# Kernel tuning notes

Hardware: AMD Instinct MI355X
Metric: run time of the kernel (lower is better)

The kernel has to match this reference:

```python
import math
import jax, jax.numpy as jnp
import numpy as np
from jax.scipy.linalg import cho_factor, cho_solve, block_diag

NUM_SENSORS = 64
T_STEPS = 2048
LOG2PI = float(np.log(2.0 * np.pi))

NCV_PROCESS_NOISE = np.array([[1.0/3.0, 0.0, 0.5, 0.0],
                              [0.0, 1.0/3.0, 0.0, 0.5],
                              [0.5, 0.0, 1.0, 0.0],
                              [0.0, 0.5, 0.0, 1.0]], dtype=np.float32)
NCV_TRANSITION_MATRIX = np.array([[1.0, 0.0, 1.0, 0.0],
                                  [0.0, 1.0, 0.0, 1.0],
                                  [0.0, 0.0, 1.0, 0.0],
                                  [0.0, 0.0, 0.0, 1.0]], dtype=np.float32)


def setup_inputs() -> dict:
    key = jax.random.key(0)
    k1, k2 = jax.random.split(key)
    track = jax.random.normal(k1, (T_STEPS, 2), dtype=jnp.float32)
    # positive covariance scales for the bias prior (torch param init ~ ones)
    bias_scales = jax.random.uniform(k2, (2,), jnp.float32, 0.5, 1.5)
    obs_noise = jnp.float32(0.7)
    trans_noise = jnp.float32(0.3)
    return {"track": track, "bias_scales": bias_scales,
            "obs_noise": obs_noise, "trans_noise": trans_noise}


def _hmm_forward(track, bias_scales, obs_noise, trans_noise, num_sensors):
    S = num_sensors
    OD = 2 * S           # obs_dim
    D = OD + 4           # augmented latent: [bias(OD); state(4)]
    T = track.shape[0]
    dt = track.dtype

    # observation matrix exactly as in torch source:
    # eye(4,2).expand(S,4,2).transpose(0,-1).reshape(4, OD)
    E = jnp.eye(4, 2, dtype=dt)
    Hobs = jnp.transpose(jnp.broadcast_to(E, (S, 4, 2)), (2, 1, 0)).reshape(4, OD)
    # augmented emission: y = bias + state @ Hobs  ->  H_aug z
    Haug = jnp.concatenate([jnp.eye(OD, dtype=dt), Hobs.T], axis=1)  # (OD, D)

    F = jnp.asarray(NCV_TRANSITION_MATRIX, dt)
    # trans scale_tril = trans_noise * chol(NCV_Q) -> cov = trans_noise^2 * NCV_Q
    Qs = (trans_noise ** 2) * jnp.asarray(NCV_PROCESS_NOISE, dt)
    A = block_diag(jnp.eye(OD, dtype=dt), F)                         # (D, D)
    Q = block_diag(jnp.zeros((OD, OD), dt), Qs)                      # (D, D)
    # obs scale_tril = obs_noise * I -> cov = obs_noise^2 * I
    R = (obs_noise ** 2) * jnp.eye(OD, dtype=dt)

    # bias prior covariance = diag(bias_scales interleaved per sensor)
    bias_var = jnp.broadcast_to(bias_scales, (S, 2)).reshape(-1)     # (OD,)
    m0 = jnp.zeros((D,), dt)
    P0 = jnp.diag(jnp.concatenate([bias_var, jnp.ones((4,), dt)]))

    # obs vector per step: x.expand(S,2).reshape(-1) (interleaved repeat)
    ys = jnp.broadcast_to(track[:, None, :], (T, S, 2)).reshape(T, OD)

    def step(carry, y):
        m, P, ll = carry
        # predict
        mp = A @ m
        Pp = A @ P @ A.T + Q
        # innovation
        HP = Haug @ Pp                      # (OD, D)
        Sm = HP @ Haug.T + R                # (OD, OD)
        cf = cho_factor(Sm, lower=True)
        v = y - Haug @ mp                   # (OD,)
        # update
        K = cho_solve(cf, HP)               # S^{-1} H Pp, (OD, D)
        m_new = mp + K.T @ v
        P_new = Pp - HP.T @ K
        P_new = 0.5 * (P_new + P_new.T)
        # log-likelihood of innovation
        logdet = 2.0 * jnp.sum(jnp.log(jnp.diag(cf[0])))
        quad = v @ cho_solve(cf, v)
        ll = ll - 0.5 * (OD * LOG2PI + logdet + quad)
        return (m_new, P_new, ll), None

    (mT, PT, ll), _ = jax.lax.scan(step, (m0, P0, jnp.zeros((), dt)), ys)
    # funsor's remaining Gaussian over (bias, state_T) has precision = inv(filtered cov)
    cfP = cho_factor(PT, lower=True)
    prec = cho_solve(cfP, jnp.eye(D, dtype=dt))
    return ll, prec


def reference(track, bias_scales, obs_noise, trans_noise):
    return _hmm_forward(track, bias_scales, obs_noise, trans_noise, NUM_SENSORS)
```

## Files before the change

kernel.cpp:

```cpp
#include <hip/hip_runtime.h>
#include <math.h>

#define L2PI 1.8378770664093454835606594728112
#define LN2  0.69314718055994530941723212145818

struct LP {
    float jFF, jFL, jFB, jLL, jLB, jBB;
    float hF, hL, hB, g, dm, de;
};

struct Cn { float qa, qb, qc, wa, wb, ri, Cstep; };

__device__ __forceinline__ float shf(float v, int s) { return __shfl(v, s, 64); }
__device__ __forceinline__ float sx (float v, int m) { return __shfl_xor(v, m, 64); }

#define LGKM0() do { \
    asm volatile("s_waitcnt lgkmcnt(0)" ::: "memory"); \
    __builtin_amdgcn_sched_barrier(0); \
} while (0)

#define OFF_S   0
#define OFF_SI  16
#define OFF_F1  32
#define OFF_F2T 48
#define OFF_MT  64
#define OFF_A1  80
#define OFF_C1T 96
#define OFF_B2T 112
#define OFF_V4  128
#define OFF_HM  132
#define GSTRIDE 152

__device__ __forceinline__ float4 ld4(const float* p) {
    return *(const float4*)p;
}
__device__ __forceinline__ float dot4(float4 a, float4 b) {
    float s = a.x * b.x;
    s = fmaf(a.y, b.y, s);
    s = fmaf(a.z, b.z, s);
    s = fmaf(a.w, b.w, s);
    return s;
}

__device__ __forceinline__ LP init_lane(float x0, float x1, const Cn& C, int i, int j) {
    LP P;
    float v = 0.0f;
    if (i == j) v = (i < 2) ? C.qa : C.qc;
    if ((i ^ j) == 2) v = C.wa;
    P.jFF = v;
    v = 0.0f;
    if (j == (i & 1))     v = (i < 2) ? -C.qa : -C.wa;
    if (j == (i & 1) + 2) v = (i < 2) ? -C.qb : -C.wb;
    P.jFL = v;
    P.jFB = 0.0f;
    v = 0.0f;
    if (i == j) v = ((i < 2) ? C.qa : C.qc) + (((i & 1) == 0) ? 2.0f*C.ri : 0.0f);
    if ((i ^ j) == 2) v = C.qb;
    P.jLL = v;
    P.jLB = (((i == 0) && (j < 2)) || ((i == 2) && (j >= 2))) ? C.ri : 0.0f;
    P.jBB = (i == j) ? C.ri : 0.0f;
    P.hF = 0.0f;
    P.hL = ((j & 1) == 0) ? C.ri * (x0 + x1) : 0.0f;
    P.hB = C.ri * ((j & 1) ? x1 : x0);
    P.g  = -C.ri * (x0*x0 + x1*x1) + C.Cstep;
    P.dm = 1.0f; P.de = 0.0f;
    return P;
}

__device__ __forceinline__ LP compose(const LP& P1, const LP& P2, float* gl, int i, int j) {
    float hm = P1.hL + P2.hF;
    float Mb = P1.jLB + P2.jFB;
    float S  = P1.jLL + P2.jFF;
    float dm = P1.dm * P2.dm;
    float de = P1.de + P2.de;
    { int ex; dm = frexpf(dm, &ex); de += (float)ex; }
    const int ij = 4*i + j, ji = 4*j + i;

    gl[OFF_S   + ij] = S;
    gl[OFF_F1  + ij] = P1.jFL;
    gl[OFF_F2T + ji] = P2.jFL;
    gl[OFF_MT  + ji] = Mb;
    if (i == 0) gl[OFF_HM + j] = hm;
    LGKM0();

    const int r0 = (j == 0) ? 1 : 0;
    const int r1 = (j <= 1) ? 2 : 1;
    const int r2 = (j <= 2) ? 3 : 2;
    float4 R0 = ld4(gl + OFF_S + 4*r0);
    float4 R1 = ld4(gl + OFF_S + 4*r1);
    float4 R2 = ld4(gl + OFF_S + 4*r2);
    float4 RJ = ld4(gl + OFF_S + 4*j);
    float4 f1r4 = ld4(gl + OFF_F1  + 4*i);
    float4 f1T4 = ld4(gl + OFF_F1  + 4*j);
    float4 f2c4 = ld4(gl + OFF_F2T + 4*j);
    float4 f2T4 = ld4(gl + OFF_F2T + 4*i);
    float4 mc4  = ld4(gl + OFF_MT  + 4*j);
    float4 mT4  = ld4(gl + OFF_MT  + 4*i);
    float4 hm4  = ld4(gl + OFF_HM);

    const bool i0 = (i == 0), i1 = (i <= 1), i2 = (i <= 2);
    float m00 = i0 ? R0.y : R0.x, m01 = i1 ? R0.z : R0.y, m02 = i2 ? R0.w : R0.z;
    float m10 = i0 ? R1.y : R1.x, m11 = i1 ? R1.z : R1.y, m12 = i2 ? R1.w : R1.z;
    float m20 = i0 ? R2.y : R2.x, m21 = i1 ? R2.z : R2.y, m22 = i2 ? R2.w : R2.z;
    float d0 = fmaf(m11, m22, -m12*m21);
    float d1 = fmaf(m10, m22, -m12*m20);
    float d2 = fmaf(m10, m21, -m11*m20);
    float det3 = m00*d0 - m01*d1 + m02*d2;
    float adj = (((i + j) & 1) ? -det3 : det3);
    float sji = (i < 2) ? (i0 ? RJ.x : RJ.y) : ((i == 2) ? RJ.z : RJ.w);
    float t = sji * adj;
    t += sx(t, 4); t += sx(t, 8);
    float det = t;
    dm *= det; { int ex; dm = frexpf(dm, &ex); de += (float)ex; }
    float Sio = adj * (1.0f / det);

    gl[OFF_SI + ij] = Sio;
    LGKM0();
    float4 sr4 = ld4(gl + OFF_SI + 4*i);
    float4 sc4 = ld4(gl + OFF_SI + 4*j);

    float A1  = dot4(f1r4, sc4);
    float C1  = dot4(sr4,  mc4);
    float B2  = dot4(sr4,  f2c4);
    float v4i = dot4(sr4,  hm4);

    gl[OFF_A1  + ij] = A1;
    gl[OFF_C1T + ji] = C1;
    gl[OFF_B2T + ji] = B2;
    if (i == j) gl[OFF_V4 + i] = v4i;
    LGKM0();
    float4 a1r4 = ld4(gl + OFF_A1  + 4*i);
    float4 a1j4 = ld4(gl + OFF_A1  + 4*j);
    float4 c1c4 = ld4(gl + OFF_C1T + 4*j);
    float4 b2c4 = ld4(gl + OFF_B2T + 4*j);
    float4 v44  = ld4(gl + OFF_V4);

    LP R;
    R.jFF = P1.jFF - dot4(a1r4, f1T4);
    R.jFL = -dot4(a1r4, f2c4);
    R.jFB = P1.jFB - dot4(a1r4, mc4);
    R.jLL = P2.jLL - dot4(f2T4, b2c4);
    R.jLB = P2.jLB - dot4(f2T4, c1c4);
    R.jBB = P1.jBB + P2.jBB - dot4(mT4, c1c4);
    R.hF  = P1.hF - dot4(a1j4, hm4);
    R.hL  = P2.hL - dot4(f2c4, v44);
    R.hB  = P1.hB + P2.hB - dot4(mc4, v44);
    R.g   = P1.g + P2.g + 2.0f*(float)L2PI + 0.5f*dot4(hm4, v44);
    R.dm = dm; R.de = de;
    return R;
}

__device__ __forceinline__ LP fetchx(const LP& P, int m) {
    LP O;
    O.jFF = sx(P.jFF,m); O.jFL = sx(P.jFL,m); O.jFB = sx(P.jFB,m);
    O.jLL = sx(P.jLL,m); O.jLB = sx(P.jLB,m); O.jBB = sx(P.jBB,m);
    O.hF  = sx(P.hF,m);  O.hL  = sx(P.hL,m);  O.hB  = sx(P.hB,m);
    O.g   = sx(P.g,m);   O.dm  = sx(P.dm,m);  O.de  = sx(P.de,m);
    return O;
}
__device__ __forceinline__ LP csel(bool up, const LP& O, const LP& P) {
    LP A;
    A.jFF = up?O.jFF:P.jFF; A.jFL = up?O.jFL:P.jFL; A.jFB = up?O.jFB:P.jFB;
    A.jLL = up?O.jLL:P.jLL; A.jLB = up?O.jLB:P.jLB; A.jBB = up?O.jBB:P.jBB;
    A.hF  = up?O.hF :P.hF;  A.hL  = up?O.hL :P.hL;  A.hB  = up?O.hB :P.hB;
    A.g   = up?O.g  :P.g;   A.dm  = up?O.dm :P.dm;  A.de  = up?O.de :P.de;
    return A;
}
__device__ __forceinline__ void pot_store(float* p, const LP& P) {
    p[0]=P.jFF; p[1]=P.jFL; p[2]=P.jFB; p[3]=P.jLL; p[4]=P.jLB; p[5]=P.jBB;
    p[6]=P.hF;  p[7]=P.hL;  p[8]=P.hB;  p[9]=P.g;   p[10]=P.dm; p[11]=P.de;
}
__device__ __forceinline__ LP pot_load(const float* p) {
    LP P;
    P.jFF=p[0]; P.jFL=p[1]; P.jFB=p[2]; P.jLL=p[3]; P.jLB=p[4]; P.jBB=p[5];
    P.hF=p[6];  P.hL=p[7];  P.hB=p[8];  P.g=p[9];   P.dm=p[10]; P.de=p[11];
    return P;
}

__global__ __launch_bounds__(512)
void hmm_produce(const float* __restrict__ track,
                 const float* __restrict__ obs_noise_p,
                 const float* __restrict__ trans_noise_p,
                 float* __restrict__ ws)
{
    __shared__ float pool[2][8][16][13];
    __shared__ __align__(16) float cbuf[32 * GSTRIDE];
    const int tid = (int)threadIdx.x;
    const int l = tid & 63, w = tid >> 6;
    const int i = (l >> 2) & 3, j = l & 3, g = (l >> 4) & 3;
    const int gid = w * 4 + g;
    float* gl = &cbuf[(size_t)gid * GSTRIDE];
    const int bid = (int)blockIdx.x;

    const double sg2d = (double)obs_noise_p[0] * (double)obs_noise_p[0];
    const double qn2d = (double)trans_noise_p[0] * (double)trans_noise_p[0];

    Cn C;
    C.qa = (float)(12.0/qn2d); C.qb = (float)(-6.0/qn2d); C.qc = (float)(4.0/qn2d);
    C.wa = (float)(6.0/qn2d);  C.wb = (float)(-2.0/qn2d);
    C.ri = (float)(32.0/sg2d);
    C.Cstep = (float)(-2.0*log(2.0*M_PI*sg2d/32.0) - 2.0*L2PI
                      - 0.5*(4.0*log(qn2d) - 2.0*log(12.0)));

    const int t0 = (bid * 32 + gid) * 2;
    LP P;
    #pragma unroll 1
    for (int op = 0; op < 6; ++op) {
        LP A, Bp;
        if (op == 0) {
            A  = init_lane(track[2*t0+0], track[2*t0+1], C, i, j);
            Bp = init_lane(track[2*t0+2], track[2*t0+3], C, i, j);
        } else if (op < 3) {
            const int m = 16 << (op - 1);
            LP O = fetchx(P, m);
            const bool up = (l & m) != 0;
            A  = csel(up, O, P);
            Bp = csel(up, P, O);
        } else {
            const int s = 1 << (op - 3);
            const int buf = (op - 3) & 1;
            if (l < 16) pot_store(&pool[buf][w][l][0], P);
            __syncthreads();
            LP O = pot_load(&pool[buf][w ^ s][l & 15][0]);
            const bool up = (w & s) != 0;
            A  = csel(up, O, P);
            Bp = csel(up, P, O);
        }
        P = compose(A, Bp, gl, i, j);
    }
    if (w == 0 && l < 16)
        pot_store(ws + ((size_t)bid * 16 + l) * 12, P);
}

__global__ __launch_bounds__(512)
void hmm_consume(const float* __restrict__ bias_scales,
                 const float* __restrict__ obs_noise_p,
                 const float* __restrict__ ws,
                 float* __restrict__ out)
{
    __shared__ float pool[2][8][16][13];
    __shared__ __align__(16) float cbuf[32 * GSTRIDE];
    __shared__ float sTi[8][8];
    __shared__ float sA[4];
    __shared__ float sLL;
    const int tid = (int)threadIdx.x;
    const int l = tid & 63, w = tid >> 6;
    const int i = (l >> 2) & 3, j = l & 3, gb = l & 48, g = (l >> 4) & 3;
    const int gid = w * 4 + g;
    float* gl = &cbuf[(size_t)gid * GSTRIDE];

    const double sg2d = (double)obs_noise_p[0] * (double)obs_noise_p[0];
    const double a00 = (double)bias_scales[0];
    const double a01 = (double)bias_scales[1];

    LP P = pot_load(ws + ((size_t)gid * 16 + (l & 15)) * 12);
    #pragma unroll 1
    for (int op = 0; op < 5; ++op) {
        LP A, Bp;
        if (op < 2) {
            const int m = 16 << op;
            LP O = fetchx(P, m);
            const bool up = (l & m) != 0;
            A  = csel(up, O, P);
            Bp = csel(up, P, O);
        } else {
            const int s = 1 << (op - 2);
            const int buf = (op - 2) & 1;
            if (l < 16) pot_store(&pool[buf][w][l][0], P);
            __syncthreads();
            LP O = pot_load(&pool[buf][w ^ s][l & 15][0]);
            const bool up = (w & s) != 0;
            A  = csel(up, O, P);
            Bp = csel(up, P, O);
        }
        P = compose(A, Bp, gl, i, j);
    }

    if (w == 0) {
        const float a0i = (float)((i & 1) ? a01 : a00);
        P.jFF += (i == j) ? 1.0f : 0.0f;
        P.jBB += (i == j) ? 32.0f / a0i : 0.0f;
        P.g   += (float)(-4.0*L2PI + 2.0*log(32.0) - log(a00) - log(a01));
        float dm = P.dm, de = P.de;
        float S = P.jFF;
        const int r0 = (j == 0) ? 1 : 0;
        const int r1 = (j <= 1) ? 2 : 1;
        const int r2 = (j <= 2) ? 3 : 2;
        const int c0 = (i == 0) ? 1 : 0;
        const int c1 = (i <= 1) ? 2 : 1;
        const int c2 = (i <= 2) ? 3 : 2;
        float m00 = shf(S, gb + 4*r0 + c0), m01 = shf(S, gb + 4*r0 + c1), m02 = shf(S, gb + 4*r0 + c2);
        float m10 = shf(S, gb + 4*r1 + c0), m11 = shf(S, gb + 4*r1 + c1), m12 = shf(S, gb + 4*r1 + c2);
        float m20 = shf(S, gb + 4*r2 + c0), m21 = shf(S, gb + 4*r2 + c1), m22 = shf(S, gb + 4*r2 + c2);
        float d0 = fmaf(m11, m22, -m12*m21);
        float d1 = fmaf(m10, m22, -m12*m20);
        float d2 = fmaf(m10, m21, -m11*m20);
        float det3 = m00*d0 - m01*d1 + m02*d2;
        float adj = (((i + j) & 1) ? -det3 : det3);
        float sji = shf(S, gb + 4*j + i);
        float tdet = sji * adj;
        tdet += sx(tdet, 4); tdet += sx(tdet, 8);
        float det = tdet;
        dm *= det; { int ex; dm = frexpf(dm, &ex); de += (float)ex; }
        const float Si = adj * (1.0f / det);
        float sr[4], fr[4], fT[4], bc[4], bT[4], hfc[4];
        #pragma unroll
        for (int r = 0; r < 4; ++r) {
            sr[r]  = shf(Si, gb + 4*i + r);
            fr[r]  = shf(P.jFL, gb + 4*r + i);
            fT[r]  = shf(P.jFL, gb + 4*r + j);
            bc[r]  = shf(P.jFB, gb + 4*r + i);
            bT[r]  = shf(P.jFB, gb + 4*r + j);
            hfc[r] = shf(P.hF, gb + 5*r);
        }
        float YL = 0.0f, YB = 0.0f, yFi = 0.0f;
        #pragma unroll
        for (int r = 0; r < 4; ++r) {
            YL  = fmaf(sr[r], fT[r], YL);
            YB  = fmaf(sr[r], bT[r], YB);
            yFi = fmaf(sr[r], hfc[r], yFi);
        }
        float ylc[4], ybc[4], yfc[4];
        #pragma unroll
        for (int r = 0; r < 4; ++r) {
            ylc[r] = shf(YL, gb + 4*r + j);
            ybc[r] = shf(YB, gb + 4*r + j);
            yfc[r] = shf(yFi, gb + 5*r);
        }
        float s1 = 0.0f, s2 = 0.0f, s3 = 0.0f, sh1 = 0.0f, sh2 = 0.0f, qF = 0.0f;
        #pragma unroll
        for (int r = 0; r < 4; ++r) {
            s1  = fmaf(fr[r], ylc[r], s1);
            s2  = fmaf(fr[r], ybc[r], s2);
            s3  = fmaf(bc[r], ybc[r], s3);
            sh1 = fmaf(fT[r], yfc[r], sh1);
            sh2 = fmaf(bT[r], yfc[r], sh2);
            qF  = fmaf(hfc[r], yfc[r], qF);
        }
        float J8ss = P.jLL - s1;
        float J8sb = P.jLB - s2;
        float J8bb = P.jBB - s3;
        float h8s  = P.hL - sh1;
        float h8b  = P.hB - sh2;
        float g8   = P.g + 2.0f*(float)L2PI + 0.5f*qF;

        const int I = l >> 3, J = l & 7, i4 = I & 3, j4 = J & 3;
        float ss  = shf(J8ss, 4*i4 + j4);
        float sb  = shf(J8sb, 4*i4 + j4);
        float sbT = shf(J8sb, 4*j4 + i4);
        float bb  = shf(J8bb, 4*i4 + j4);
        float A8 = (I < 4) ? ((J < 4) ? ss : sb) : ((J < 4) ? sbT : bb);
        const float J8sav = A8;
        float h8v = (J < 4) ? shf(h8s, j4) : shf(h8b, j4);
        float h8r = (I < 4) ? shf(h8s, i4) : shf(h8b, i4);
        float K8 = (I == J) ? 1.0f : 0.0f;
        #pragma unroll 1
        for (int p = 0; p < 8; ++p) {
            float piv = shf(A8, 9*p);
            dm *= piv; { int ex; dm = frexpf(dm, &ex); de += (float)ex; }
            float ip = 1.0f / piv;
            float Ap = shf(A8, 8*p + J) * ip;
            float Kp = shf(K8, 8*p + J) * ip;
            float f  = shf(A8, 8*I + p);
            bool isp = (I == p);
            A8 = isp ? A8 * ip : fmaf(-f, Ap, A8);
            K8 = isp ? K8 * ip : fmaf(-f, Kp, K8);
        }
        float tq = h8r * K8 * h8v;
        tq += sx(tq,1); tq += sx(tq,2); tq += sx(tq,4);
        tq += sx(tq,8); tq += sx(tq,16); tq += sx(tq,32);

        double ll = (double)g8 + 4.0*L2PI
                    - 0.5*(log((double)dm) + (double)de*LN2) + 0.5*(double)tq;
        const double Td = 2048.0;
        const double c0d = sg2d/a00, c1d = sg2d/a01;
        ll += -31.0*(Td*(L2PI + log(sg2d)) + log((c0d+Td)/c0d))
              -31.0*(Td*(L2PI + log(sg2d)) + log((c1d+Td)/c1d))
              -2.0*Td*log(32.0);

        const float i32 = 1.0f/32.0f, irn = 0.176776695296637f;
        int a = (I >= 4) ? I - 4 : I + 4;
        int b = (J >= 4) ? J - 4 : J + 4;
        float scale = (I >= 4 && J >= 4) ? i32 : (((I >= 4) != (J >= 4)) ? irn : 1.0f);
        sTi[a][b] = J8sav * scale;
        if (l < 4) {
            double a0k = (l & 1) ? a01 : a00;
            sA[l] = (float)(a0k*sg2d/(sg2d + Td*a0k));
        }
        if (l == 0) sLL = (float)ll;
    }
    __syncthreads();

    const float inv32 = 1.0f/32.0f;
    const float invrn = 0.176776695296637f;
    const int total = 1 + 132*132;
    #pragma unroll 1
    for (int idx = tid; idx < total; idx += 512) {
        float v;
        if (idx == 0) {
            v = sLL;
        } else {
            int el = idx - 1;
            int r = el / 132;
            int cc = el - 132*r;
            if (r < 128) {
                int ki = ((r >> 6) << 1) | (r & 1);
                if (cc < 128) {
                    int kj = ((cc >> 6) << 1) | (cc & 1);
                    v = sTi[ki][kj] * inv32;
                    if (ki == kj) {
                        float ia = 1.0f / sA[ki];
                        v -= ia * inv32;
                        if (r == cc) v += ia;
                    }
                } else {
                    v = sTi[ki][cc - 124] * invrn;
                }
            } else {
                if (cc < 128) {
                    int kj = ((cc >> 6) << 1) | (cc & 1);
                    v = sTi[kj][r - 124] * invrn;
                } else {
                    v = sTi[r - 124][cc - 124];
                }
            }
        }
        out[idx] = v;
    }
}

extern "C" void kernel_launch(void* const* d_in, const int* in_sizes, int n_in,
                              void* d_out, int out_size, void* d_ws, size_t ws_size,
                              hipStream_t stream) {
    (void)in_sizes; (void)n_in; (void)out_size; (void)ws_size;
    const float* track       = (const float*)d_in[0];
    const float* bias_scales = (const float*)d_in[1];
    const float* obs_noise   = (const float*)d_in[2];
    const float* trans_noise = (const float*)d_in[3];
    float* out = (float*)d_out;
    float* ws  = (float*)d_ws;
    hipLaunchKernelGGL(hmm_produce, dim3(32), dim3(512), 0, stream,
                       track, obs_noise, trans_noise, ws);
    hipLaunchKernelGGL(hmm_consume, dim3(1), dim3(512), 0, stream,
                       bias_scales, obs_noise, ws, out);
}
```

Before: 87.48 us.

## Compute full 4x4 inverse redundantly per lane to drop LDS round-trips

Each lane now computes the full 4x4 adjugate and inverse of the Schur block from one LDS read, instead of computing one cofactor per lane and exchanging intermediates through LDS with waitcnt barriers. This removes two LDS store/wait/load phases from compose and the cross-lane shuffles in the final elimination. The cost is much more redundant per-lane arithmetic (16 3x3 determinants and several 4x4 matrix-vector products) and higher register pressure.

New measurement: 88.83 us. Within noise of the previous version (+1.5%).

```diff
diff --git a/kernel.cpp b/kernel.cpp
--- a/kernel.cpp
+++ b/kernel.cpp
@@ -20,15 +20,10 @@
 } while (0)
 
 #define OFF_S   0
-#define OFF_SI  16
-#define OFF_F1  32
-#define OFF_F2T 48
-#define OFF_MT  64
-#define OFF_A1  80
-#define OFF_C1T 96
-#define OFF_B2T 112
-#define OFF_V4  128
-#define OFF_HM  132
+#define OFF_F1  16
+#define OFF_F2T 32
+#define OFF_MT  48
+#define OFF_HM  64
 #define GSTRIDE 152
 
 __device__ __forceinline__ float4 ld4(const float* p) {
@@ -40,6 +35,49 @@
     s = fmaf(a.z, b.z, s);
     s = fmaf(a.w, b.w, s);
     return s;
+}
+__device__ __forceinline__ float sel4(float x0, float x1, float x2, float x3, int k) {
+    return (k == 0) ? x0 : ((k == 1) ? x1 : ((k == 2) ? x2 : x3));
+}
+
+struct Adj4 { float e[4][4]; };
+__device__ __forceinline__ Adj4 adj4(const float4& Ra, const float4& Rb,
+                                     const float4& Rc, const float4& Rd) {
+    float sS[4][4];
+    sS[0][0]=Ra.x; sS[0][1]=Ra.y; sS[0][2]=Ra.z; sS[0][3]=Ra.w;
+    sS[1][0]=Rb.x; sS[1][1]=Rb.y; sS[1][2]=Rb.z; sS[1][3]=Rb.w;
+    sS[2][0]=Rc.x; sS[2][1]=Rc.y; sS[2][2]=Rc.z; sS[2][3]=Rc.w;
+    sS[3][0]=Rd.x; sS[3][1]=Rd.y; sS[3][2]=Rd.z; sS[3][3]=Rd.w;
+    Adj4 A;
+    #pragma unroll
+    for (int a = 0; a < 4; ++a) {
+        const int c0 = (a == 0) ? 1 : 0;
+        const int c1 = (a <= 1) ? 2 : 1;
+        const int c2 = (a <= 2) ? 3 : 2;
+        #pragma unroll
+        for (int b = 0; b < 4; ++b) {
+            const int r0 = (b == 0) ? 1 : 0;
+            const int r1 = (b <= 1) ? 2 : 1;
+            const int r2 = (b <= 2) ? 3 : 2;
+            float m00 = sS[r0][c0], m01 = sS[r0][c1], m02 = sS[r0][c2];
+            float m10 = sS[r1][c0], m11 = sS[r1][c1], m12 = sS[r1][c2];
+            float m20 = sS[r2][c0], m21 = sS[r2][c1], m22 = sS[r2][c2];
+            float d0 = fmaf(m11, m22, -m12*m21);
+            float d1 = fmaf(m10, m22, -m12*m20);
+            float d2 = fmaf(m10, m21, -m11*m20);
+            float det3 = m00*d0 - m01*d1 + m02*d2;
+            A.e[a][b] = (((a + b) & 1) ? -det3 : det3);
+        }
+    }
+    return A;
+}
+__device__ __forceinline__ float det4_colj(const Adj4& A, const float4& RJ, int j) {
+    float a0j = sel4(A.e[0][0], A.e[0][1], A.e[0][2], A.e[0][3], j);
+    float a1j = sel4(A.e[1][0], A.e[1][1], A.e[1][2], A.e[1][3], j);
+    float a2j = sel4(A.e[2][0], A.e[2][1], A.e[2][2], A.e[2][3], j);
+    float a3j = sel4(A.e[3][0], A.e[3][1], A.e[3][2], A.e[3][3], j);
+    float t0 = RJ.x * a0j, t1 = RJ.y * a1j, t2 = RJ.z * a2j, t3 = RJ.w * a3j;
+    return (t0 + t1) + (t2 + t3);
 }
 
 __device__ __forceinline__ LP init_lane(float x0, float x1, const Cn& C, int i, int j) {
@@ -82,13 +120,10 @@
     gl[OFF_MT  + ji] = Mb;
     if (i == 0) gl[OFF_HM + j] = hm;
     LGKM0();
-
-    const int r0 = (j == 0) ? 1 : 0;
-    const int r1 = (j <= 1) ? 2 : 1;
-    const int r2 = (j <= 2) ? 3 : 2;
-    float4 R0 = ld4(gl + OFF_S + 4*r0);
-    float4 R1 = ld4(gl + OFF_S + 4*r1);
-    float4 R2 = ld4(gl + OFF_S + 4*r2);
+    float4 Ra = ld4(gl + OFF_S + 0);
+    float4 Rb = ld4(gl + OFF_S + 4);
+    float4 Rc = ld4(gl + OFF_S + 8);
+    float4 Rd = ld4(gl + OFF_S + 12);
     float4 RJ = ld4(gl + OFF_S + 4*j);
     float4 f1r4 = ld4(gl + OFF_F1  + 4*i);
     float4 f1T4 = ld4(gl + OFF_F1  + 4*j);
@@ -98,42 +133,25 @@
     float4 mT4  = ld4(gl + OFF_MT  + 4*i);
     float4 hm4  = ld4(gl + OFF_HM);
 
-    const bool i0 = (i == 0), i1 = (i <= 1), i2 = (i <= 2);
-    float m00 = i0 ? R0.y : R0.x, m01 = i1 ? R0.z : R0.y, m02 = i2 ? R0.w : R0.z;
-    float m10 = i0 ? R1.y : R1.x, m11 = i1 ? R1.z : R1.y, m12 = i2 ? R1.w : R1.z;
-    float m20 = i0 ? R2.y : R2.x, m21 = i1 ? R2.z : R2.y, m22 = i2 ? R2.w : R2.z;
-    float d0 = fmaf(m11, m22, -m12*m21);
-    float d1 = fmaf(m10, m22, -m12*m20);
-    float d2 = fmaf(m10, m21, -m11*m20);
-    float det3 = m00*d0 - m01*d1 + m02*d2;
-    float adj = (((i + j) & 1) ? -det3 : det3);
-    float sji = (i < 2) ? (i0 ? RJ.x : RJ.y) : ((i == 2) ? RJ.z : RJ.w);
-    float t = sji * adj;
-    t += sx(t, 4); t += sx(t, 8);
-    float det = t;
+    Adj4 A = adj4(Ra, Rb, Rc, Rd);
+    float det = det4_colj(A, RJ, j);
     dm *= det; { int ex; dm = frexpf(dm, &ex); de += (float)ex; }
-    float Sio = adj * (1.0f / det);
-
-    gl[OFF_SI + ij] = Sio;
-    LGKM0();
-    float4 sr4 = ld4(gl + OFF_SI + 4*i);
-    float4 sc4 = ld4(gl + OFF_SI + 4*j);
-
-    float A1  = dot4(f1r4, sc4);
-    float C1  = dot4(sr4,  mc4);
-    float B2  = dot4(sr4,  f2c4);
-    float v4i = dot4(sr4,  hm4);
-
-    gl[OFF_A1  + ij] = A1;
-    gl[OFF_C1T + ji] = C1;
-    gl[OFF_B2T + ji] = B2;
-    if (i == j) gl[OFF_V4 + i] = v4i;
-    LGKM0();
-    float4 a1r4 = ld4(gl + OFF_A1  + 4*i);
-    float4 a1j4 = ld4(gl + OFF_A1  + 4*j);
-    float4 c1c4 = ld4(gl + OFF_C1T + 4*j);
-    float4 b2c4 = ld4(gl + OFF_B2T + 4*j);
-    float4 v44  = ld4(gl + OFF_V4);
+    const float rdet = 1.0f / det;
+    float4 sie0 = make_float4(A.e[0][0]*rdet, A.e[0][1]*rdet, A.e[0][2]*rdet, A.e[0][3]*rdet);
+    float4 sie1 = make_float4(A.e[1][0]*rdet, A.e[1][1]*rdet, A.e[1][2]*rdet, A.e[1][3]*rdet);
+    float4 sie2 = make_float4(A.e[2][0]*rdet, A.e[2][1]*rdet, A.e[2][2]*rdet, A.e[2][3]*rdet);
+    float4 sie3 = make_float4(A.e[3][0]*rdet, A.e[3][1]*rdet, A.e[3][2]*rdet, A.e[3][3]*rdet);
+
+    float4 a1r4 = make_float4(dot4(f1r4, sie0), dot4(f1r4, sie1),
+                              dot4(f1r4, sie2), dot4(f1r4, sie3));
+    float4 a1j4 = make_float4(dot4(f1T4, sie0), dot4(f1T4, sie1),
+                              dot4(f1T4, sie2), dot4(f1T4, sie3));
+    float4 c1c4 = make_float4(dot4(sie0, mc4), dot4(sie1, mc4),
+                              dot4(sie2, mc4), dot4(sie3, mc4));
+    float4 b2c4 = make_float4(dot4(sie0, f2c4), dot4(sie1, f2c4),
+                              dot4(sie2, f2c4), dot4(sie3, f2c4));
+    float4 v44  = make_float4(dot4(sie0, hm4), dot4(sie1, hm4),
+                              dot4(sie2, hm4), dot4(sie3, hm4));
 
     LP R;
     R.jFF = P1.jFF - dot4(a1r4, f1T4);
@@ -282,61 +300,46 @@
         P.jBB += (i == j) ? 32.0f / a0i : 0.0f;
         P.g   += (float)(-4.0*L2PI + 2.0*log(32.0) - log(a00) - log(a01));
         float dm = P.dm, de = P.de;
-        float S = P.jFF;
-        const int r0 = (j == 0) ? 1 : 0;
-        const int r1 = (j <= 1) ? 2 : 1;
-        const int r2 = (j <= 2) ? 3 : 2;
-        const int c0 = (i == 0) ? 1 : 0;
-        const int c1 = (i <= 1) ? 2 : 1;
-        const int c2 = (i <= 2) ? 3 : 2;
-        float m00 = shf(S, gb + 4*r0 + c0), m01 = shf(S, gb + 4*r0 + c1), m02 = shf(S, gb + 4*r0 + c2);
-        float m10 = shf(S, gb + 4*r1 + c0), m11 = shf(S, gb + 4*r1 + c1), m12 = shf(S, gb + 4*r1 + c2);
-        float m20 = shf(S, gb + 4*r2 + c0), m21 = shf(S, gb + 4*r2 + c1), m22 = shf(S, gb + 4*r2 + c2);
-        float d0 = fmaf(m11, m22, -m12*m21);
-        float d1 = fmaf(m10, m22, -m12*m20);
-        float d2 = fmaf(m10, m21, -m11*m20);
-        float det3 = m00*d0 - m01*d1 + m02*d2;
-        float adj = (((i + j) & 1) ? -det3 : det3);
-        float sji = shf(S, gb + 4*j + i);
-        float tdet = sji * adj;
-        tdet += sx(tdet, 4); tdet += sx(tdet, 8);
-        float det = tdet;
+        const int ij = 4*i + j, ji = 4*j + i;
+
+        gl[OFF_S   + ij] = P.jFF;
+        gl[OFF_F1  + ji] = P.jFL;
+        gl[OFF_F2T + ji] = P.jFB;
+        if (i == 0) gl[OFF_HM + j] = P.hF;
+        LGKM0();
+        float4 Ra = ld4(gl + OFF_S + 0);
+        float4 Rb = ld4(gl + OFF_S + 4);
+        float4 Rc = ld4(gl + OFF_S + 8);
+        float4 Rd = ld4(gl + OFF_S + 12);
+        float4 RJ = ld4(gl + OFF_S + 4*j);
+        float4 fr4 = ld4(gl + OFF_F1  + 4*i);
+        float4 fT4 = ld4(gl + OFF_F1  + 4*j);
+        float4 bc4 = ld4(gl + OFF_F2T + 4*i);
+        float4 bT4 = ld4(gl + OFF_F2T + 4*j);
+        float4 hf4 = ld4(gl + OFF_HM);
+
+        Adj4 A = adj4(Ra, Rb, Rc, Rd);
+        float det = det4_colj(A, RJ, j);
         dm *= det; { int ex; dm = frexpf(dm, &ex); de += (float)ex; }
-        const float Si = adj * (1.0f / det);
-        float sr[4], fr[4], fT[4], bc[4], bT[4], hfc[4];
-        #pragma unroll
-        for (int r = 0; r < 4; ++r) {
-            sr[r]  = shf(Si, gb + 4*i + r);
-            fr[r]  = shf(P.jFL, gb + 4*r + i);
-            fT[r]  = shf(P.jFL, gb + 4*r + j);
-            bc[r]  = shf(P.jFB, gb + 4*r + i);
-            bT[r]  = shf(P.jFB, gb + 4*r + j);
-            hfc[r] = shf(P.hF, gb + 5*r);
-        }
-        float YL = 0.0f, YB = 0.0f, yFi = 0.0f;
-        #pragma unroll
-        for (int r = 0; r < 4; ++r) {
-            YL  = fmaf(sr[r], fT[r], YL);
-            YB  = fmaf(sr[r], bT[r], YB);
-            yFi = fmaf(sr[r], hfc[r], yFi);
-        }
-        float ylc[4], ybc[4], yfc[4];
-        #pragma unroll
-        for (int r = 0; r < 4; ++r) {
-            ylc[r] = shf(YL, gb + 4*r + j);
-            ybc[r] = shf(YB, gb + 4*r + j);
-            yfc[r] = shf(yFi, gb + 5*r);
-        }
-        float s1 = 0.0f, s2 = 0.0f, s3 = 0.0f, sh1 = 0.0f, sh2 = 0.0f, qF = 0.0f;
-        #pragma unroll
-        for (int r = 0; r < 4; ++r) {
-            s1  = fmaf(fr[r], ylc[r], s1);
-            s2  = fmaf(fr[r], ybc[r], s2);
-            s3  = fmaf(bc[r], ybc[r], s3);
-            sh1 = fmaf(fT[r], yfc[r], sh1);
-            sh2 = fmaf(bT[r], yfc[r], sh2);
-            qF  = fmaf(hfc[r], yfc[r], qF);
-        }
+        const float rdet = 1.0f / det;
+        float4 sie0 = make_float4(A.e[0][0]*rdet, A.e[0][1]*rdet, A.e[0][2]*rdet, A.e[0][3]*rdet);
+        float4 sie1 = make_float4(A.e[1][0]*rdet, A.e[1][1]*rdet, A.e[1][2]*rdet, A.e[1][3]*rdet);
+        float4 sie2 = make_float4(A.e[2][0]*rdet, A.e[2][1]*rdet, A.e[2][2]*rdet, A.e[2][3]*rdet);
+        float4 sie3 = make_float4(A.e[3][0]*rdet, A.e[3][1]*rdet, A.e[3][2]*rdet, A.e[3][3]*rdet);
+
+        float4 ylc4 = make_float4(dot4(sie0, fT4), dot4(sie1, fT4),
+                                  dot4(sie2, fT4), dot4(sie3, fT4));
+        float4 ybc4 = make_float4(dot4(sie0, bT4), dot4(sie1, bT4),
+                                  dot4(sie2, bT4), dot4(sie3, bT4));
+        float4 yfc4 = make_float4(dot4(sie0, hf4), dot4(sie1, hf4),
+                                  dot4(sie2, hf4), dot4(sie3, hf4));
+        float s1  = dot4(fr4, ylc4);
+        float s2  = dot4(fr4, ybc4);
+        float s3  = dot4(bc4, ybc4);
+        float sh1 = dot4(fT4, yfc4);
+        float sh2 = dot4(bT4, yfc4);
+        float qF  = dot4(hf4, yfc4);
+
         float J8ss = P.jLL - s1;
         float J8sb = P.jLB - s2;
         float J8bb = P.jBB - s3;
```
